# Performance work log

Hardware: AMD Instinct MI355X
Metric: run time of the kernel (lower is better)

Reference implementation:

```python
import jax, jax.numpy as jnp
import numpy as np

NUM_TYPES = 1000  # num_edge_type (static for segment_sum)


def setup_inputs() -> dict:
    key = jax.random.key(0)
    k1, k2, k3, k4, k5 = jax.random.split(key, 5)
    N = 1_000_000          # batch of edges
    D = 256                # embed_size
    ATTR_NUM = 200_000     # base_node_num - c_num - e_num
    TOTAL_ATTRS = 50_000   # sum of ragged attr-list lengths over types (~50/type)
    data = jax.random.randint(k1, (N,), 0, NUM_TYPES, dtype=jnp.int64) if jax.config.jax_enable_x64 else jax.random.randint(k1, (N,), 0, NUM_TYPES, dtype=jnp.int32)
    attr_table = jax.random.normal(k2, (ATTR_NUM, D), dtype=jnp.float32)
    edge_type_embedding = jax.random.normal(k3, (NUM_TYPES, D), dtype=jnp.float32)
    flat_attr_ids = jax.random.randint(k4, (TOTAL_ATTRS,), 0, ATTR_NUM, dtype=jnp.int32)
    attr_seg_ids = jax.random.randint(k5, (TOTAL_ATTRS,), 0, NUM_TYPES, dtype=jnp.int32)
    return {
        "data": data,
        "attr_table": attr_table,
        "edge_type_embedding": edge_type_embedding,
        "flat_attr_ids": flat_attr_ids,
        "attr_seg_ids": attr_seg_ids,
    }


def reference(data, attr_table, edge_type_embedding, flat_attr_ids, attr_seg_ids):
    # Per-type bag-sum of attribute embeddings (ragged gather + segment reduce).
    # type_attr_sum[t] == sum_{a in type2attr[t]} attr_emb[a]; empty types -> 0,
    # which matches the original's self.zero_attr fallback.
    gathered = attr_table[flat_attr_ids]                          # [T_attrs, D]
    type_attr_sum = jax.ops.segment_sum(gathered, attr_seg_ids,
                                        num_segments=NUM_TYPES)   # [NUM_TYPES, D]
    # fusion_type == 'add': edge-type embedding + summed attr embeddings per edge
    return edge_type_embedding[data] + type_attr_sum[data]        # [N, D]
```

## Files before the change

kernel.cpp:

```cpp
#include <hip/hip_runtime.h>


#define EE_D4     64
#define EE_NT     1000
#define EE_K      4

typedef float        fvec4 __attribute__((ext_vector_type(4)));
typedef unsigned int uvec2 __attribute__((ext_vector_type(2)));

__device__ __forceinline__ unsigned int ee_pack_bf16(float a, float b) {
    unsigned int ua = __builtin_bit_cast(unsigned int, a);
    unsigned int ub = __builtin_bit_cast(unsigned int, b);
    ua = (ua + 0x7FFFu + ((ua >> 16) & 1u)) >> 16;
    ub = (ub + 0x7FFFu + ((ub >> 16) & 1u)) >> 16;
    return ua | (ub << 16);
}

template <int SL>
__global__ __launch_bounds__(256) void ee_build_part(
        const fvec4* __restrict__ attr,
        const int* __restrict__ ids,
        const int* __restrict__ segs,
        fvec4* __restrict__ part, int na) {
    const int t0    = blockIdx.x * EE_K;
    const int slice = blockIdx.y;
    const int tid   = threadIdx.x;
    const int wave  = tid >> 6;
    const int lane  = tid & 63;

    const int chunk = (na + SL - 1) / SL;
    const int s0 = slice * chunk;
    const int s1 = (s0 + chunk < na) ? s0 + chunk : na;

    fvec4 acc[EE_K];
    #pragma unroll
    for (int k = 0; k < EE_K; ++k) acc[k] = (fvec4)0.f;

    for (int base = s0 + wave * 64; base < s1; base += 256) {
        int a = base + lane;
        int s = -1, id = 0;
        if (a < s1) { s = segs[a]; id = ids[a]; }
        #pragma unroll
        for (int k = 0; k < EE_K; ++k) {
            unsigned long long m = __ballot(s == t0 + k);
            while (m) {
                int j = __ffsll((long long)m) - 1;
                m &= m - 1;
                int aid = __shfl(id, j);
                acc[k] += attr[(size_t)aid * EE_D4 + lane];
            }
        }
    }

    __shared__ fvec4 red[EE_K][4][64];
    #pragma unroll
    for (int k = 0; k < EE_K; ++k) red[k][wave][lane] = acc[k];
    __syncthreads();
    if (wave < EE_K) {
        int k = wave;
        fvec4 r = red[k][0][lane];
        #pragma unroll
        for (int w = 1; w < 4; ++w) r += red[k][w][lane];
        part[((size_t)slice * EE_NT + (t0 + k)) * EE_D4 + lane] = r;
    }
}

template <int SL>
__global__ __launch_bounds__(256) void ee_finalize(
        const fvec4* __restrict__ part,
        const fvec4* __restrict__ ete,
        uvec2* __restrict__ comb) {
    const int t    = blockIdx.x * EE_K + (threadIdx.x >> 6);
    const int lane = threadIdx.x & 63;
    fvec4 r = ete[(size_t)t * EE_D4 + lane];
    #pragma unroll
    for (int s = 0; s < SL; ++s)
        r += part[((size_t)s * EE_NT + t) * EE_D4 + lane];
    uvec2 p;
    p.x = ee_pack_bf16(r.x, r.y);
    p.y = ee_pack_bf16(r.z, r.w);
    comb[(size_t)t * EE_D4 + lane] = p;
}

__device__ __forceinline__ fvec4 ee_unpack(uvec2 q) {
    fvec4 v;
    v.x = __builtin_bit_cast(float, q.x << 16);
    v.y = __builtin_bit_cast(float, q.x & 0xFFFF0000u);
    v.z = __builtin_bit_cast(float, q.y << 16);
    v.w = __builtin_bit_cast(float, q.y & 0xFFFF0000u);
    return v;
}

__global__ __launch_bounds__(256) void ee_gather_out(
        const int* __restrict__ data,
        const uvec2* __restrict__ comb,
        fvec4* __restrict__ out, int n) {
    const int gid  = blockIdx.x * blockDim.x + threadIdx.x;
    const int wave = gid >> 6;
    const int lane = gid & 63;
    const int nw   = (gridDim.x * blockDim.x) >> 6;

    for (int base = wave * 64; base < n; base += nw * 64) {
        int r = base + lane;
        int idx = (r < n) ? __builtin_nontemporal_load(&data[r]) : 0;
        int lim = n - base;
        if (lim >= 64) {
            #pragma unroll
            for (int j = 0; j < 64; ++j) {
                int t = __builtin_amdgcn_readlane(idx, j);
                uvec2 q = comb[(size_t)t * EE_D4 + lane];
                __builtin_nontemporal_store(ee_unpack(q), &out[(size_t)(base + j) * EE_D4 + lane]);
            }
        } else {
            for (int j = 0; j < lim; ++j) {
                int t = __shfl(idx, j);
                uvec2 q = comb[(size_t)t * EE_D4 + lane];
                __builtin_nontemporal_store(ee_unpack(q), &out[(size_t)(base + j) * EE_D4 + lane]);
            }
        }
    }
}

extern "C" void kernel_launch(void* const* d_in, const int* in_sizes, int n_in,
                              void* d_out, int out_size, void* d_ws, size_t ws_size,
                              hipStream_t stream) {
    const int*   data          = (const int*)d_in[0];
    const float* attr_table    = (const float*)d_in[1];
    const float* ete           = (const float*)d_in[2];
    const int*   flat_attr_ids = (const int*)d_in[3];
    const int*   attr_seg_ids  = (const int*)d_in[4];
    int N  = in_sizes[0];
    int TA = in_sizes[3];

    char*  ws   = (char*)d_ws;
    uvec2* comb = (uvec2*)ws;
    fvec4* part = (fvec4*)(ws + (512 << 10));
    const size_t partBytes = (size_t)EE_NT * EE_D4 * sizeof(fvec4);

    if (ws_size >= (512 << 10) + 8 * partBytes) {
        dim3 grid(EE_NT / EE_K, 8);
        ee_build_part<8><<<grid, 256, 0, stream>>>(
            (const fvec4*)attr_table, flat_attr_ids, attr_seg_ids, part, TA);
        ee_finalize<8><<<EE_NT / EE_K, 256, 0, stream>>>(part, (const fvec4*)ete, comb);
    } else {
        dim3 grid(EE_NT / EE_K, 4);
        ee_build_part<4><<<grid, 256, 0, stream>>>(
            (const fvec4*)attr_table, flat_attr_ids, attr_seg_ids, part, TA);
        ee_finalize<4><<<EE_NT / EE_K, 256, 0, stream>>>(part, (const fvec4*)ete, comb);
    }

    ee_gather_out<<<2048, 256, 0, stream>>>(
        data, comb, (fvec4*)d_out, N);
}
```

Before: 208.9 us.

## Replace ballot-based per-type scan with LDS atomic segment-sum build kernel

Adds a build kernel that splits the embedding dimension into 16 column chunks and the attribute list into 8 slices. Each block keeps all 1000 types for its 16 columns in a 64KB LDS table and scatter-adds gathered attribute values with LDS atomics. This removes the old scheme's repeated scanning of the full id/segment arrays by every group of 4 types. In exchange only 128 blocks launch, each running a long serial loop of dependent global loads with little parallelism, and LDS atomic contention is added.

```diff
diff --git a/kernel.cpp b/kernel.cpp
--- a/kernel.cpp
+++ b/kernel.cpp
@@ -4,6 +4,8 @@
 #define EE_D4     64
 #define EE_NT     1000
 #define EE_K      4
+#define EE_NSL    8
+#define EE_NCH    16
 
 typedef float        fvec4 __attribute__((ext_vector_type(4)));
 typedef unsigned int uvec2 __attribute__((ext_vector_type(2)));
@@ -14,6 +16,39 @@
     ua = (ua + 0x7FFFu + ((ua >> 16) & 1u)) >> 16;
     ub = (ub + 0x7FFFu + ((ub >> 16) & 1u)) >> 16;
     return ua | (ub << 16);
+}
+
+__global__ __launch_bounds__(256) void ee_build_lds(
+        const float* __restrict__ attr,
+        const int* __restrict__ ids,
+        const int* __restrict__ segs,
+        float* __restrict__ part, int na) {
+    const int c     = blockIdx.x;
+    const int slice = blockIdx.y;
+    const int tid   = threadIdx.x;
+    const int sub   = tid & 15;
+    const int slot  = tid >> 4;
+
+    __shared__ float lds[EE_NT * 16];
+    for (int i = tid; i < EE_NT * 16; i += 256) lds[i] = 0.f;
+    __syncthreads();
+
+    const int chunk = (na + EE_NSL - 1) / EE_NSL;
+    const int s0 = slice * chunk;
+    const int s1 = (s0 + chunk < na) ? s0 + chunk : na;
+
+    for (int e = s0 + slot; e < s1; e += 16) {
+        int t  = segs[e];
+        int id = ids[e];
+        float v = attr[(size_t)id * 256 + c * 16 + sub];
+        atomicAdd(&lds[t * 16 + sub], v);
+    }
+    __syncthreads();
+
+    for (int i = tid; i < EE_NT * 16; i += 256) {
+        int t = i >> 4, s2 = i & 15;
+        part[((size_t)slice * EE_NT + t) * 256 + c * 16 + s2] = lds[i];
+    }
 }
 
 template <int SL>
@@ -137,14 +172,12 @@
     fvec4* part = (fvec4*)(ws + (512 << 10));
     const size_t partBytes = (size_t)EE_NT * EE_D4 * sizeof(fvec4);
 
-    if (ws_size >= (512 << 10) + 8 * partBytes) {
-        dim3 grid(EE_NT / EE_K, 8);
-        ee_build_part<8><<<grid, 256, 0, stream>>>(
-            (const fvec4*)attr_table, flat_attr_ids, attr_seg_ids, part, TA);
-        ee_finalize<8><<<EE_NT / EE_K, 256, 0, stream>>>(part, (const fvec4*)ete, comb);
+    if (ws_size >= (512 << 10) + EE_NSL * partBytes) {
+        ee_build_lds<<<dim3(EE_NCH, EE_NSL), 256, 0, stream>>>(
+            attr_table, flat_attr_ids, attr_seg_ids, (float*)part, TA);
+        ee_finalize<EE_NSL><<<EE_NT / EE_K, 256, 0, stream>>>(part, (const fvec4*)ete, comb);
     } else {
-        dim3 grid(EE_NT / EE_K, 4);
-        ee_build_part<4><<<grid, 256, 0, stream>>>(
+        ee_build_part<4><<<dim3(EE_NT / EE_K, 4), 256, 0, stream>>>(
             (const fvec4*)attr_table, flat_attr_ids, attr_seg_ids, part, TA);
         ee_finalize<4><<<EE_NT / EE_K, 256, 0, stream>>>(part, (const fvec4*)ete, comb);
     }
```

After: 412.6 us. 97.5% more time.
